# Kernel optimization log

Hardware: AMD Instinct MI355X
Metric: run time of the kernel (lower is better)

The kernel has to match this reference:

```python
import jax, jax.numpy as jnp
import numpy as np

NEG_SLOPE = 0.01  # nn.LeakyReLU default
NUM_GRAPHS = 64


def leaky_relu(x):
    return jnp.where(x >= 0, x, NEG_SLOPE * x)


def gcn_conv(x, edge_index, W, b):
    """PyG GCNConv: add self-loops, symmetric norm, aggregate, + bias."""
    n = x.shape[0]
    h = x @ W  # [N, F]
    loop = jnp.arange(n, dtype=edge_index.dtype)
    src = jnp.concatenate([edge_index[0], loop])
    dst = jnp.concatenate([edge_index[1], loop])
    deg = jax.ops.segment_sum(jnp.ones_like(dst, dtype=h.dtype), dst, num_segments=n)
    dinv = jnp.where(deg > 0, deg ** -0.5, 0.0)
    norm = dinv[src] * dinv[dst]  # [E+N]
    msg = h[src] * norm[:, None]  # [E+N, F] dominant intermediate
    out = jax.ops.segment_sum(msg, dst, num_segments=n)
    return out + b


def gep(x, batch, num_graphs):
    """global mean pool over batch segment ids."""
    s = jax.ops.segment_sum(x, batch, num_segments=num_graphs)
    cnt = jax.ops.segment_sum(jnp.ones(x.shape[0], dtype=x.dtype), batch, num_segments=num_graphs)
    return s / jnp.maximum(cnt, 1.0)[:, None]


def setup_inputs() -> dict:
    key = jax.random.key(0)
    ks = jax.random.split(key, 16)
    N, E, F, D, B = 10000, 80000, 1024, 128, NUM_GRAPHS
    sc = 1.0 / np.sqrt(F)
    inp = {
        "pro1_x": jax.random.normal(ks[0], (N, F), jnp.float32),
        "pro1_edge_index": jax.random.randint(ks[1], (2, E), 0, N, jnp.int64),
        "pro1_batch": jnp.sort(jax.random.randint(ks[2], (N,), 0, B, jnp.int64)),
        "pro2_x": jax.random.normal(ks[3], (N, F), jnp.float32),
        "pro2_edge_index": jax.random.randint(ks[4], (2, E), 0, N, jnp.int64),
        "pro2_batch": jnp.sort(jax.random.randint(ks[5], (N,), 0, B, jnp.int64)),
        "mas1_straight": 0, "mas1_flipped": 0, "mas2_straight": 0, "mas2_flipped": 0,
        "conv1_W": jax.random.normal(ks[6], (F, F), jnp.float32) * sc,
        "conv1_b": jnp.zeros((F,), jnp.float32),
        "fc1_W": jax.random.normal(ks[7], (F, D), jnp.float32) * sc,
        "fc1_b": jnp.zeros((D,), jnp.float32),
        "conv2_W": jax.random.normal(ks[8], (F, F), jnp.float32) * sc,
        "conv2_b": jnp.zeros((F,), jnp.float32),
        "fc2_W": jax.random.normal(ks[9], (F, D), jnp.float32) * sc,
        "fc2_b": jnp.zeros((D,), jnp.float32),
        "final_W": jax.random.normal(ks[10], (2 * D, 1), jnp.float32) * (1.0 / np.sqrt(2 * D)),
        "final_b": jnp.zeros((1,), jnp.float32),
    }
    return inp


def reference(pro1_x, pro1_edge_index, pro1_batch, pro2_x, pro2_edge_index, pro2_batch,
              mas1_straight, mas1_flipped, mas2_straight, mas2_flipped,
              conv1_W, conv1_b, fc1_W, fc1_b, conv2_W, conv2_b, fc2_W, fc2_b,
              final_W, final_b):
    # branch 1 (dropout = identity at inference)
    x = leaky_relu(gcn_conv(pro1_x, pro1_edge_index, conv1_W, conv1_b))
    x = gep(x, pro1_batch, NUM_GRAPHS)
    x = leaky_relu(x @ fc1_W + fc1_b)
    # branch 2
    xt = leaky_relu(gcn_conv(pro2_x, pro2_edge_index, conv2_W, conv2_b))
    xt = gep(xt, pro2_batch, NUM_GRAPHS)
    xt = leaky_relu(xt @ fc2_W + fc2_b)
    combined = jnp.concatenate([x, xt], axis=1)  # [B, 256]
    return combined @ final_W + final_b  # [B, 1]
```

## Files before the change

kernel.cpp:

```cpp
#include <hip/hip_runtime.h>
#include <cstdint>
#include <cstddef>

#define FDIM 1024
#define DDIM 128
#define NGRAPH 64
#define FCH 8
#define QN 4
#define FILLB 320

#define AS1 __attribute__((address_space(1)))
#define AS3 __attribute__((address_space(3)))

typedef float f32x4 __attribute__((ext_vector_type(4)));
typedef short s16x8 __attribute__((ext_vector_type(8)));

__device__ __forceinline__ unsigned short f2bf(float f) {
  unsigned int x = __float_as_uint(f);
  unsigned int r = (x + 0x7fffu + ((x >> 16) & 1u)) >> 16;
  return (unsigned short)r;
}
__device__ __forceinline__ float bflo(unsigned int v) {
  return __uint_as_float(v << 16);
}
__device__ __forceinline__ float bfhi(unsigned int v) {
  return __uint_as_float(v & 0xffff0000u);
}

__device__ __forceinline__ int lower_bound(const int* a, int n, int v) {
  int lo = 0, hi = n;
  while (lo < hi) {
    int mid = (lo + hi) >> 1;
    if (a[mid] < v) lo = mid + 1; else hi = mid;
  }
  return lo;
}
__global__ __launch_bounds__(256) void k_init(int* deg1, int* deg2,
                                              const int* __restrict__ batch1,
                                              const int* __restrict__ batch2,
                                              int* cnt1, int* gstart1,
                                              int* cnt2, int* gstart2, int N) {
  int bid = blockIdx.x, t = threadIdx.x;
  if (bid < 40) {
    int i = bid * 256 + t;
    if (i < N) deg1[i] = 1;
  } else if (bid < 80) {
    int i = (bid - 40) * 256 + t;
    if (i < N) deg2[i] = 1;
  } else {
    if (t < 128) {
      const int* batch = (t < NGRAPH) ? batch1 : batch2;
      int* cnt = (t < NGRAPH) ? cnt1 : cnt2;
      int* gstart = (t < NGRAPH) ? gstart1 : gstart2;
      int g = t & (NGRAPH - 1);
      int lo = lower_bound(batch, N, g);
      int hi = lower_bound(batch, N, g + 1);
      gstart[g] = lo;
      cnt[g] = hi - lo;
    }
  }
}

__global__ __launch_bounds__(256) void k_prep_cast(const int* __restrict__ ei1,
                                                   const int* __restrict__ ei2,
                                                   int* deg1, int* deg2,
                                                   const float4* __restrict__ x1,
                                                   const float4* __restrict__ x2,
                                                   const float* __restrict__ W1,
                                                   const float* __restrict__ W2,
                                                   ushort4* xb1, ushort4* xb2,
                                                   unsigned short* Wt1, unsigned short* Wt2,
                                                   int E, int n4, int gE, int nxb) {
  __shared__ unsigned short tile[64][65];
  int br = blockIdx.y;
  int x = blockIdx.x, t = threadIdx.x;
  if (x < gE) {
    const int* ei = br ? ei2 : ei1;
    int* deg = br ? deg2 : deg1;
    int i = x * 256 + t;
    if (i < E) atomicAdd(&deg[ei[E + i]], 1);
  } else if (x < gE + nxb) {
    const float4* xx = br ? x2 : x1;
    ushort4* xb = br ? xb2 : xb1;
    int i = (x - gE) * 256 + t;
    if (i < n4) {
      float4 v = xx[i];
      ushort4 o;
      o.x = f2bf(v.x); o.y = f2bf(v.y); o.z = f2bf(v.z); o.w = f2bf(v.w);
      xb[i] = o;
    }
  } else {
    const float* W = br ? W2 : W1;
    unsigned short* Wt = br ? Wt2 : Wt1;
    int tid16 = x - gE - nxb;
    int kb = tid16 >> 4, nb = tid16 & 15;
    int tn = t & 63, tg = t >> 6;
    #pragma unroll
    for (int r = 0; r < 16; ++r) {
      int kk = tg * 16 + r;
      tile[kk][tn] = f2bf(W[(size_t)(kb * 64 + kk) * FDIM + nb * 64 + tn]);
    }
    __syncthreads();
    #pragma unroll
    for (int r = 0; r < 16; ++r) {
      int nn = tg * 16 + r;
      Wt[(size_t)(nb * 64 + nn) * FDIM + kb * 64 + tn] = tile[tn][nn];
    }
  }
}

#define SCAN_T 1024
#define SCAN_PER 16
__global__ __launch_bounds__(SCAN_T) void k_scan(const int* __restrict__ deg1,
                                                 const int* __restrict__ deg2,
                                                 int* off1, int* off2,
                                                 int* cur1, int* cur2,
                                                 float* dinv1, float* dinv2, int n) {
  const int* deg = blockIdx.x ? deg2 : deg1;
  int* off = blockIdx.x ? off2 : off1;
  int* cur = blockIdx.x ? cur2 : cur1;
  float* dinv = blockIdx.x ? dinv2 : dinv1;
  __shared__ int sums[SCAN_T];
  int t = threadIdx.x;
  int base = t * SCAN_PER;
  int local[SCAN_PER];
  int s = 0;
  #pragma unroll
  for (int i = 0; i < SCAN_PER; ++i) {
    int idx = base + i;
    int d = (idx < n) ? deg[idx] : 0;
    local[i] = s;
    s += d;
    if (idx < n) dinv[idx] = rsqrtf((float)d);
  }
  sums[t] = s;
  __syncthreads();
  for (int o = 1; o < SCAN_T; o <<= 1) {
    int v = (t >= o) ? sums[t - o] : 0;
    __syncthreads();
    sums[t] += v;
    __syncthreads();
  }
  int basesum = (t > 0) ? sums[t - 1] : 0;
  #pragma unroll
  for (int i = 0; i < SCAN_PER; ++i) {
    int idx = base + i;
    if (idx < n) { int o = basesum + local[i]; off[idx] = o; cur[idx] = o; }
  }
  if (t == SCAN_T - 1) off[n] = sums[SCAN_T - 1];
}

__global__ __launch_bounds__(256) void k_fill_gemm(const int* __restrict__ ei1,
                                                   const int* __restrict__ ei2,
                                                   int* cur1, int* cur2,
                                                   const float* __restrict__ dinv1,
                                                   const float* __restrict__ dinv2,
                                                   int* adjsrc1, int* adjsrc2,
                                                   float* adjw1, float* adjw2,
                                                   const unsigned short* __restrict__ A1,
                                                   const unsigned short* __restrict__ A2,
                                                   const unsigned short* __restrict__ B1,
                                                   const unsigned short* __restrict__ B2,
                                                   unsigned short* __restrict__ C1,
                                                   unsigned short* __restrict__ C2,
                                                   int E, int N, int M) {
  __shared__ unsigned short sm[8192];
  int br = blockIdx.y;
  if (blockIdx.x < FILLB) {
    const int* ei = br ? ei2 : ei1;
    int* cur = br ? cur2 : cur1;
    const float* dinv = br ? dinv2 : dinv1;
    int* adjsrc = br ? adjsrc2 : adjsrc1;
    float* adjw = br ? adjw2 : adjw1;
    int i = blockIdx.x * 256 + threadIdx.x;
    if (i < E) {
      int s = ei[i];
      int d = ei[E + i];
      int p = atomicAdd(&cur[d], 1);
      adjsrc[p] = s;
      adjw[p] = dinv[s] * dinv[d];
    }
    if (i < N) {
      int p = atomicAdd(&cur[i], 1);
      adjsrc[p] = i;
      adjw[p] = dinv[i] * dinv[i];
    }
    return;
  }
  const unsigned short* A = br ? A2 : A1;
  const unsigned short* Bt = br ? B2 : B1;
  unsigned short* C = br ? C2 : C1;
  const int K = FDIM;
  int tid = threadIdx.x;
  int w = tid >> 6, lane = tid & 63;
  int wm = w >> 1, wn = w & 1;

  int bx = blockIdx.x - FILLB;
  int per_xcd = (gridDim.x - FILLB) >> 3;
  int l = (bx & 7) * per_xcd + (bx >> 3);
  int m0 = (l >> 3) * 128;
  int n0 = (l & 7) * 128;

  int sub = lane >> 2;
  int kq = lane & 3;

  f32x4 acc[4][4];
  #pragma unroll
  for (int i = 0; i < 4; ++i)
    #pragma unroll
    for (int j = 0; j < 4; ++j)
      acc[i][j] = (f32x4){0.f, 0.f, 0.f, 0.f};

  for (int k0 = 0; k0 < K; k0 += 32) {
    #pragma unroll
    for (int j = 0; j < 2; ++j) {
      int chunk = w * 2 + j;
      int ra = m0 + chunk * 16 + sub;
      if (ra > M - 1) ra = M - 1;
      const unsigned short* ga = A + (size_t)ra * K + k0 + kq * 8;
      __builtin_amdgcn_global_load_lds((const AS1 unsigned int*)ga,
                                       (AS3 unsigned int*)&sm[chunk * 512], 16, 0, 0);
      int rb = n0 + chunk * 16 + sub;
      const unsigned short* gb = Bt + (size_t)rb * K + k0 + kq * 8;
      __builtin_amdgcn_global_load_lds((const AS1 unsigned int*)gb,
                                       (AS3 unsigned int*)&sm[4096 + chunk * 512], 16, 0, 0);
    }
    __syncthreads();
    s16x8 af[4], bfr[4];
    #pragma unroll
    for (int i = 0; i < 4; ++i) {
      int rowa = wm * 64 + i * 16 + (lane & 15);
      af[i] = *(const s16x8*)&sm[rowa * 32 + (lane >> 4) * 8];
      int rowb = wn * 64 + i * 16 + (lane & 15);
      bfr[i] = *(const s16x8*)&sm[4096 + rowb * 32 + (lane >> 4) * 8];
    }
    #pragma unroll
    for (int i = 0; i < 4; ++i)
      #pragma unroll
      for (int j = 0; j < 4; ++j)
        acc[i][j] = __builtin_amdgcn_mfma_f32_16x16x32_bf16(af[i], bfr[j], acc[i][j], 0, 0, 0);
    __syncthreads();
  }

  #pragma unroll
  for (int i = 0; i < 4; ++i) {
    int row_base = m0 + wm * 64 + i * 16 + (lane >> 4) * 4;
    #pragma unroll
    for (int j = 0; j < 4; ++j) {
      int col = n0 + wn * 64 + j * 16 + (lane & 15);
      #pragma unroll
      for (int r = 0; r < 4; ++r) {
        int row = row_base + r;
        if (row < M) C[(size_t)row * FDIM + col] = f2bf(acc[i][j][r]);
      }
    }
  }
}

__global__ __launch_bounds__(256) void k_aggpool(const unsigned short* __restrict__ h1,
                                                 const unsigned short* __restrict__ h2,
                                                 const int* __restrict__ off1,
                                                 const int* __restrict__ off2,
                                                 const int* __restrict__ adjsrc1,
                                                 const int* __restrict__ adjsrc2,
                                                 const float* __restrict__ adjw1,
                                                 const float* __restrict__ adjw2,
                                                 const float* __restrict__ bias1,
                                                 const float* __restrict__ bias2,
                                                 const int* __restrict__ cnt1,
                                                 const int* __restrict__ cnt2,
                                                 const int* __restrict__ gstart1,
                                                 const int* __restrict__ gstart2,
                                                 float* pool4_1, float* pool4_2) {
  int br = blockIdx.y;
  const unsigned short* h = br ? h2 : h1;
  const int* off = br ? off2 : off1;
  const int* adjsrc = br ? adjsrc2 : adjsrc1;
  const float* adjw = br ? adjw2 : adjw1;
  const float* bias = br ? bias2 : bias1;
  const int* cnt = br ? cnt2 : cnt1;
  const int* gstart = br ? gstart2 : gstart1;
  float* pool4 = br ? pool4_2 : pool4_1;

  int x = blockIdx.x;
  int chunk = x & (FCH - 1);
  int r = x >> 3;
  int g = r & (NGRAPH - 1);
  int q = r >> 6;

  int t = threadIdx.x;
  int grp = t >> 6, lane = t & 63;

  int n = cnt[g];
  int start = gstart[g];
  int per = (n + QN - 1) / QN;
  int v0 = start + q * per;
  int v1 = min(start + n, v0 + per);

  int colbase = chunk * 128 + lane * 2;
  const unsigned short* hc = h + colbase;
  float2 b2 = *(const float2*)(bias + colbase);
  float s0 = 0.f, s1 = 0.f;

  for (int v = v0 + grp; v < v1; v += 4) {
    int pb = off[v], pe = off[v + 1];
    float a0 = 0.f, a1 = 0.f;
    for (int pbb = pb; pbb < pe; pbb += 64) {
      int m = min(64, pe - pbb);
      int lp = pbb + ((lane < m) ? lane : (m - 1));
      int vs = adjsrc[lp];
      float vw = adjw[lp];
      int j = 0;
      for (; j + 4 <= m; j += 4) {
        int i0 = __shfl(vs, j),     i1 = __shfl(vs, j + 1);
        int i2 = __shfl(vs, j + 2), i3 = __shfl(vs, j + 3);
        float w0 = __shfl(vw, j),     w1 = __shfl(vw, j + 1);
        float w2 = __shfl(vw, j + 2), w3 = __shfl(vw, j + 3);
        unsigned int h0 = *(const unsigned int*)(hc + ((size_t)i0 << 10));
        unsigned int hv1 = *(const unsigned int*)(hc + ((size_t)i1 << 10));
        unsigned int hv2 = *(const unsigned int*)(hc + ((size_t)i2 << 10));
        unsigned int hv3 = *(const unsigned int*)(hc + ((size_t)i3 << 10));
        a0 += w0 * bflo(h0);  a1 += w0 * bfhi(h0);
        a0 += w1 * bflo(hv1); a1 += w1 * bfhi(hv1);
        a0 += w2 * bflo(hv2); a1 += w2 * bfhi(hv2);
        a0 += w3 * bflo(hv3); a1 += w3 * bfhi(hv3);
      }
      for (; j < m; ++j) {
        int i0 = __shfl(vs, j);
        float w0 = __shfl(vw, j);
        unsigned int h0 = *(const unsigned int*)(hc + ((size_t)i0 << 10));
        a0 += w0 * bflo(h0);
        a1 += w0 * bfhi(h0);
      }
    }
    a0 += b2.x; a1 += b2.y;
    s0 += (a0 >= 0.f) ? a0 : 0.01f * a0;
    s1 += (a1 >= 0.f) ? a1 : 0.01f * a1;
  }

  __shared__ float sm[4][128];
  sm[grp][lane * 2] = s0;
  sm[grp][lane * 2 + 1] = s1;
  __syncthreads();
  if (t < 128) {
    float sum = sm[0][t] + sm[1][t] + sm[2][t] + sm[3][t];
    float ic = 1.0f / fmaxf((float)n, 1.0f);
    pool4[((size_t)(q * NGRAPH + g)) * FDIM + chunk * 128 + t] = sum * ic;
  }
}

__global__ __launch_bounds__(DDIM) void k_fc(const float* __restrict__ pool4_1,
                                             const float* __restrict__ pool4_2,
                                             const float* __restrict__ W1,
                                             const float* __restrict__ W2,
                                             const float* __restrict__ b1,
                                             const float* __restrict__ b2,
                                             float* out1, float* out2) {
  const float* pool4 = blockIdx.y ? pool4_2 : pool4_1;
  const float* W = blockIdx.y ? W2 : W1;
  const float* b = blockIdx.y ? b2 : b1;
  float* out = blockIdx.y ? out2 : out1;
  int g = blockIdx.x;
  int j = threadIdx.x;
  __shared__ float xs[FDIM];
  for (int k = j; k < FDIM; k += DDIM) {
    float v = 0.f;
    #pragma unroll
    for (int q = 0; q < QN; ++q)
      v += pool4[((size_t)(q * NGRAPH + g)) * FDIM + k];
    xs[k] = v;
  }
  __syncthreads();
  float acc = b[j];
  for (int k = 0; k < FDIM; ++k) acc += xs[k] * W[(size_t)k * DDIM + j];
  out[g * DDIM + j] = (acc >= 0.f) ? acc : 0.01f * acc;
}

__global__ __launch_bounds__(DDIM) void k_final(const float* __restrict__ o1,
                                                const float* __restrict__ o2,
                                                const float* __restrict__ W,
                                                const float* __restrict__ b,
                                                float* __restrict__ out) {
  int g = blockIdx.x;
  int t = threadIdx.x;
  float acc = o1[g * DDIM + t] * W[t] + o2[g * DDIM + t] * W[DDIM + t];
  #pragma unroll
  for (int o = 32; o > 0; o >>= 1) acc += __shfl_down(acc, o);
  __shared__ float ws2[2];
  if ((t & 63) == 0) ws2[t >> 6] = acc;
  __syncthreads();
  if (t == 0) out[g] = ws2[0] + ws2[1] + b[0];
}

extern "C" void kernel_launch(void* const* d_in, const int* in_sizes, int n_in,
                              void* d_out, int out_size, void* d_ws, size_t ws_size,
                              hipStream_t stream) {
  const float* x1 = (const float*)d_in[0];
  const int* ei1 = (const int*)d_in[1];
  const int* batch1 = (const int*)d_in[2];
  const float* x2 = (const float*)d_in[3];
  const int* ei2 = (const int*)d_in[4];
  const int* batch2 = (const int*)d_in[5];
  const float* conv1_W = (const float*)d_in[10];
  const float* conv1_b = (const float*)d_in[11];
  const float* fc1_W = (const float*)d_in[12];
  const float* fc1_b = (const float*)d_in[13];
  const float* conv2_W = (const float*)d_in[14];
  const float* conv2_b = (const float*)d_in[15];
  const float* fc2_W = (const float*)d_in[16];
  const float* fc2_b = (const float*)d_in[17];
  const float* final_W = (const float*)d_in[18];
  const float* final_b = (const float*)d_in[19];
  float* out = (float*)d_out;

  const int N = in_sizes[2];
  const int E = in_sizes[1] / 2;
  const int A = E + N;

  size_t off_b = 0;
  auto alloc = [&](size_t bytes) -> void* {
    void* p = (char*)d_ws + off_b;
    off_b += (bytes + 255) & ~(size_t)255;
    return p;
  };
  unsigned short* xbf1 = (unsigned short*)alloc((size_t)N * FDIM * 2);
  unsigned short* xbf2 = (unsigned short*)alloc((size_t)N * FDIM * 2);
  unsigned short* hbf1 = (unsigned short*)alloc((size_t)N * FDIM * 2);
  unsigned short* hbf2 = (unsigned short*)alloc((size_t)N * FDIM * 2);
  unsigned short* Wt1 = (unsigned short*)alloc((size_t)FDIM * FDIM * 2);
  unsigned short* Wt2 = (unsigned short*)alloc((size_t)FDIM * FDIM * 2);
  int* deg1 = (int*)alloc(N * 4);
  int* deg2 = (int*)alloc(N * 4);
  int* cnt1 = (int*)alloc(NGRAPH * 4);
  int* cnt2 = (int*)alloc(NGRAPH * 4);
  int* gstart1 = (int*)alloc(NGRAPH * 4);
  int* gstart2 = (int*)alloc(NGRAPH * 4);
  int* off1 = (int*)alloc((N + 1) * 4);
  int* off2 = (int*)alloc((N + 1) * 4);
  int* cur1 = (int*)alloc(N * 4);
  int* cur2 = (int*)alloc(N * 4);
  float* dinv1 = (float*)alloc(N * 4);
  float* dinv2 = (float*)alloc(N * 4);
  int* adjsrc1 = (int*)alloc((size_t)A * 4);
  int* adjsrc2 = (int*)alloc((size_t)A * 4);
  float* adjw1 = (float*)alloc((size_t)A * 4);
  float* adjw2 = (float*)alloc((size_t)A * 4);
  float* pool4_1 = (float*)alloc((size_t)QN * NGRAPH * FDIM * 4);
  float* pool4_2 = (float*)alloc((size_t)QN * NGRAPH * FDIM * 4);
  float* fco1 = (float*)alloc(NGRAPH * DDIM * 4);
  float* fco2 = (float*)alloc(NGRAPH * DDIM * 4);

  const int T = 256;
  int gE = (E + T - 1) / T;
  int n4 = N * FDIM / 4;
  int nxb = (n4 + T - 1) / T;
  int mt = (N + 127) / 128;
  dim3 gPrepCast(gE + nxb + 256, 2);
  dim3 gFillGemm(FILLB + mt * 8, 2);
  dim3 gAgg(FCH * NGRAPH * QN, 2);
  dim3 gFc(NGRAPH, 2);

  k_init<<<81, T, 0, stream>>>(deg1, deg2, batch1, batch2,
                               cnt1, gstart1, cnt2, gstart2, N);
  k_prep_cast<<<gPrepCast, T, 0, stream>>>(ei1, ei2, deg1, deg2,
                                           (const float4*)x1, (const float4*)x2,
                                           conv1_W, conv2_W,
                                           (ushort4*)xbf1, (ushort4*)xbf2, Wt1, Wt2,
                                           E, n4, gE, nxb);
  k_scan<<<2, SCAN_T, 0, stream>>>(deg1, deg2, off1, off2, cur1, cur2, dinv1, dinv2, N);
  k_fill_gemm<<<gFillGemm, T, 0, stream>>>(ei1, ei2, cur1, cur2, dinv1, dinv2,
                                           adjsrc1, adjsrc2, adjw1, adjw2,
                                           xbf1, xbf2, Wt1, Wt2, hbf1, hbf2,
                                           E, N, N);
  k_aggpool<<<gAgg, T, 0, stream>>>(hbf1, hbf2, off1, off2, adjsrc1, adjsrc2,
                                    adjw1, adjw2, conv1_b, conv2_b,
                                    cnt1, cnt2, gstart1, gstart2, pool4_1, pool4_2);
  k_fc<<<gFc, DDIM, 0, stream>>>(pool4_1, pool4_2, fc1_W, fc2_W, fc1_b, fc2_b, fco1, fco2);
  k_final<<<NGRAPH, DDIM, 0, stream>>>(fco1, fco2, final_W, final_b, out);
}
```

Baseline: 334.4 us.

## Enlarge GEMM tiles, fuse fc+final, fold init into scan, widen cast

The bf16 MFMA GEMM moves from 128x128x32 tiles to 256x128x64 tiles with 8x4 accumulators per wave and a larger LDS buffer, raising data reuse per global load. The k_init kernel is replaced by memsets plus a third scan block that computes graph boundaries, with the self-loop degree added inside the scan. The fc and final kernels are fused into one launch, and the x cast now writes 8 bf16 values per thread. This cuts launches and intermediate buffers, at the cost of higher register and LDS pressure in the GEMM that may reduce occupancy.

New measurement: 341.3 us. +2.1%, slower.

```diff
diff --git a/kernel.cpp b/kernel.cpp
--- a/kernel.cpp
+++ b/kernel.cpp
@@ -9,11 +9,16 @@
 #define QN 4
 #define FILLB 320
 
+#define BM 256
+#define BN 128
+#define BK 64
+
 #define AS1 __attribute__((address_space(1)))
 #define AS3 __attribute__((address_space(3)))
 
 typedef float f32x4 __attribute__((ext_vector_type(4)));
 typedef short s16x8 __attribute__((ext_vector_type(8)));
+typedef unsigned short u16x8 __attribute__((ext_vector_type(8)));
 
 __device__ __forceinline__ unsigned short f2bf(float f) {
   unsigned int x = __float_as_uint(f);
@@ -34,31 +39,6 @@
     if (a[mid] < v) lo = mid + 1; else hi = mid;
   }
   return lo;
-}
-__global__ __launch_bounds__(256) void k_init(int* deg1, int* deg2,
-                                              const int* __restrict__ batch1,
-                                              const int* __restrict__ batch2,
-                                              int* cnt1, int* gstart1,
-                                              int* cnt2, int* gstart2, int N) {
-  int bid = blockIdx.x, t = threadIdx.x;
-  if (bid < 40) {
-    int i = bid * 256 + t;
-    if (i < N) deg1[i] = 1;
-  } else if (bid < 80) {
-    int i = (bid - 40) * 256 + t;
-    if (i < N) deg2[i] = 1;
-  } else {
-    if (t < 128) {
-      const int* batch = (t < NGRAPH) ? batch1 : batch2;
-      int* cnt = (t < NGRAPH) ? cnt1 : cnt2;
-      int* gstart = (t < NGRAPH) ? gstart1 : gstart2;
-      int g = t & (NGRAPH - 1);
-      int lo = lower_bound(batch, N, g);
-      int hi = lower_bound(batch, N, g + 1);
-      gstart[g] = lo;
-      cnt[g] = hi - lo;
-    }
-  }
 }
 
 __global__ __launch_bounds__(256) void k_prep_cast(const int* __restrict__ ei1,
@@ -68,9 +48,9 @@
                                                    const float4* __restrict__ x2,
                                                    const float* __restrict__ W1,
                                                    const float* __restrict__ W2,
-                                                   ushort4* xb1, ushort4* xb2,
+                                                   u16x8* xb1, u16x8* xb2,
                                                    unsigned short* Wt1, unsigned short* Wt2,
-                                                   int E, int n4, int gE, int nxb) {
+                                                   int E, int n8, int gE, int nxb) {
   __shared__ unsigned short tile[64][65];
   int br = blockIdx.y;
   int x = blockIdx.x, t = threadIdx.x;
@@ -81,12 +61,14 @@
     if (i < E) atomicAdd(&deg[ei[E + i]], 1);
   } else if (x < gE + nxb) {
     const float4* xx = br ? x2 : x1;
-    ushort4* xb = br ? xb2 : xb1;
+    u16x8* xb = br ? xb2 : xb1;
     int i = (x - gE) * 256 + t;
-    if (i < n4) {
-      float4 v = xx[i];
-      ushort4 o;
-      o.x = f2bf(v.x); o.y = f2bf(v.y); o.z = f2bf(v.z); o.w = f2bf(v.w);
+    if (i < n8) {
+      float4 v0 = xx[2 * i];
+      float4 v1 = xx[2 * i + 1];
+      u16x8 o;
+      o[0] = f2bf(v0.x); o[1] = f2bf(v0.y); o[2] = f2bf(v0.z); o[3] = f2bf(v0.w);
+      o[4] = f2bf(v1.x); o[5] = f2bf(v1.y); o[6] = f2bf(v1.z); o[7] = f2bf(v1.w);
       xb[i] = o;
     }
   } else {
@@ -115,7 +97,25 @@
                                                  const int* __restrict__ deg2,
                                                  int* off1, int* off2,
                                                  int* cur1, int* cur2,
-                                                 float* dinv1, float* dinv2, int n) {
+                                                 float* dinv1, float* dinv2,
+                                                 const int* __restrict__ batch1,
+                                                 const int* __restrict__ batch2,
+                                                 int* cnt1, int* gstart1,
+                                                 int* cnt2, int* gstart2, int n) {
+  if (blockIdx.x == 2) {
+    int t = threadIdx.x;
+    if (t < 128) {
+      const int* batch = (t < NGRAPH) ? batch1 : batch2;
+      int* cnt = (t < NGRAPH) ? cnt1 : cnt2;
+      int* gstart = (t < NGRAPH) ? gstart1 : gstart2;
+      int g = t & (NGRAPH - 1);
+      int lo = lower_bound(batch, n, g);
+      int hi = lower_bound(batch, n, g + 1);
+      gstart[g] = lo;
+      cnt[g] = hi - lo;
+    }
+    return;
+  }
   const int* deg = blockIdx.x ? deg2 : deg1;
   int* off = blockIdx.x ? off2 : off1;
   int* cur = blockIdx.x ? cur2 : cur1;
@@ -128,7 +128,7 @@
   #pragma unroll
   for (int i = 0; i < SCAN_PER; ++i) {
     int idx = base + i;
-    int d = (idx < n) ? deg[idx] : 0;
+    int d = (idx < n) ? (deg[idx] + 1) : 0;
     local[i] = s;
     s += d;
     if (idx < n) dinv[idx] = rsqrtf((float)d);
@@ -150,21 +150,21 @@
   if (t == SCAN_T - 1) off[n] = sums[SCAN_T - 1];
 }
 
-__global__ __launch_bounds__(256) void k_fill_gemm(const int* __restrict__ ei1,
-                                                   const int* __restrict__ ei2,
-                                                   int* cur1, int* cur2,
-                                                   const float* __restrict__ dinv1,
-                                                   const float* __restrict__ dinv2,
-                                                   int* adjsrc1, int* adjsrc2,
-                                                   float* adjw1, float* adjw2,
-                                                   const unsigned short* __restrict__ A1,
-                                                   const unsigned short* __restrict__ A2,
-                                                   const unsigned short* __restrict__ B1,
-                                                   const unsigned short* __restrict__ B2,
-                                                   unsigned short* __restrict__ C1,
-                                                   unsigned short* __restrict__ C2,
-                                                   int E, int N, int M) {
-  __shared__ unsigned short sm[8192];
+__global__ __launch_bounds__(256, 2) void k_fill_gemm(const int* __restrict__ ei1,
+                                                      const int* __restrict__ ei2,
+                                                      int* cur1, int* cur2,
+                                                      const float* __restrict__ dinv1,
+                                                      const float* __restrict__ dinv2,
+                                                      int* adjsrc1, int* adjsrc2,
+                                                      float* adjw1, float* adjw2,
+                                                      const unsigned short* __restrict__ A1,
+                                                      const unsigned short* __restrict__ A2,
+                                                      const unsigned short* __restrict__ B1,
+                                                      const unsigned short* __restrict__ B2,
+                                                      unsigned short* __restrict__ C1,
+                                                      unsigned short* __restrict__ C2,
+                                                      int E, int N, int M) {
+  __shared__ unsigned short sm[24576];
   int br = blockIdx.y;
   if (blockIdx.x < FILLB) {
     const int* ei = br ? ei2 : ei1;
@@ -198,53 +198,61 @@
   int bx = blockIdx.x - FILLB;
   int per_xcd = (gridDim.x - FILLB) >> 3;
   int l = (bx & 7) * per_xcd + (bx >> 3);
-  int m0 = (l >> 3) * 128;
-  int n0 = (l & 7) * 128;
-
-  int sub = lane >> 2;
-  int kq = lane & 3;
-
-  f32x4 acc[4][4];
+  int m0 = (l >> 3) * BM;
+  int n0 = (l & 7) * BN;
+
+  int seg_r = lane >> 3;
+  int seg_c = lane & 7;
+
+  f32x4 acc[8][4];
   #pragma unroll
-  for (int i = 0; i < 4; ++i)
+  for (int i = 0; i < 8; ++i)
     #pragma unroll
     for (int j = 0; j < 4; ++j)
       acc[i][j] = (f32x4){0.f, 0.f, 0.f, 0.f};
 
-  for (int k0 = 0; k0 < K; k0 += 32) {
-    #pragma unroll
-    for (int j = 0; j < 2; ++j) {
-      int chunk = w * 2 + j;
-      int ra = m0 + chunk * 16 + sub;
+  for (int k0 = 0; k0 < K; k0 += BK) {
+    #pragma unroll
+    for (int c = 0; c < 8; ++c) {
+      int ra = m0 + c * 32 + w * 8 + seg_r;
       if (ra > M - 1) ra = M - 1;
-      const unsigned short* ga = A + (size_t)ra * K + k0 + kq * 8;
+      const unsigned short* ga = A + (size_t)ra * K + k0 + seg_c * 8;
       __builtin_amdgcn_global_load_lds((const AS1 unsigned int*)ga,
-                                       (AS3 unsigned int*)&sm[chunk * 512], 16, 0, 0);
-      int rb = n0 + chunk * 16 + sub;
-      const unsigned short* gb = Bt + (size_t)rb * K + k0 + kq * 8;
+                                       (AS3 unsigned int*)&sm[c * 2048 + w * 512], 16, 0, 0);
+    }
+    #pragma unroll
+    for (int c = 0; c < 4; ++c) {
+      int rb = n0 + c * 32 + w * 8 + seg_r;
+      const unsigned short* gb = Bt + (size_t)rb * K + k0 + seg_c * 8;
       __builtin_amdgcn_global_load_lds((const AS1 unsigned int*)gb,
-                                       (AS3 unsigned int*)&sm[4096 + chunk * 512], 16, 0, 0);
+                                       (AS3 unsigned int*)&sm[16384 + c * 2048 + w * 512], 16, 0, 0);
     }
     __syncthreads();
-    s16x8 af[4], bfr[4];
-    #pragma unroll
-    for (int i = 0; i < 4; ++i) {
-      int rowa = wm * 64 + i * 16 + (lane & 15);
-      af[i] = *(const s16x8*)&sm[rowa * 32 + (lane >> 4) * 8];
-      int rowb = wn * 64 + i * 16 + (lane & 15);
-      bfr[i] = *(const s16x8*)&sm[4096 + rowb * 32 + (lane >> 4) * 8];
-    }
-    #pragma unroll
-    for (int i = 0; i < 4; ++i)
+    #pragma unroll
+    for (int kk = 0; kk < 2; ++kk) {
+      s16x8 af[8], bfr[4];
       #pragma unroll
-      for (int j = 0; j < 4; ++j)
-        acc[i][j] = __builtin_amdgcn_mfma_f32_16x16x32_bf16(af[i], bfr[j], acc[i][j], 0, 0, 0);
+      for (int i = 0; i < 8; ++i) {
+        int rowa = wm * 128 + i * 16 + (lane & 15);
+        af[i] = *(const s16x8*)&sm[rowa * 64 + kk * 32 + (lane >> 4) * 8];
+      }
+      #pragma unroll
+      for (int j = 0; j < 4; ++j) {
+        int rowb = wn * 64 + j * 16 + (lane & 15);
+        bfr[j] = *(const s16x8*)&sm[16384 + rowb * 64 + kk * 32 + (lane >> 4) * 8];
+      }
+      #pragma unroll
+      for (int i = 0; i < 8; ++i)
+        #pragma unroll
+        for (int j = 0; j < 4; ++j)
+          acc[i][j] = __builtin_amdgcn_mfma_f32_16x16x32_bf16(af[i], bfr[j], acc[i][j], 0, 0, 0);
+    }
     __syncthreads();
   }
 
   #pragma unroll
-  for (int i = 0; i < 4; ++i) {
-    int row_base = m0 + wm * 64 + i * 16 + (lane >> 4) * 4;
+  for (int i = 0; i < 8; ++i) {
+    int row_base = m0 + wm * 128 + i * 16 + (lane >> 4) * 4;
     #pragma unroll
     for (int j = 0; j < 4; ++j) {
       int col = n0 + wn * 64 + j * 16 + (lane & 15);
@@ -349,47 +357,41 @@
   }
 }
 
-__global__ __launch_bounds__(DDIM) void k_fc(const float* __restrict__ pool4_1,
-                                             const float* __restrict__ pool4_2,
-                                             const float* __restrict__ W1,
-                                             const float* __restrict__ W2,
-                                             const float* __restrict__ b1,
-                                             const float* __restrict__ b2,
-                                             float* out1, float* out2) {
-  const float* pool4 = blockIdx.y ? pool4_2 : pool4_1;
-  const float* W = blockIdx.y ? W2 : W1;
-  const float* b = blockIdx.y ? b2 : b1;
-  float* out = blockIdx.y ? out2 : out1;
+__global__ __launch_bounds__(256) void k_fc_final(const float* __restrict__ pool4_1,
+                                                  const float* __restrict__ pool4_2,
+                                                  const float* __restrict__ W1,
+                                                  const float* __restrict__ W2,
+                                                  const float* __restrict__ b1,
+                                                  const float* __restrict__ b2,
+                                                  const float* __restrict__ fW,
+                                                  const float* __restrict__ fb,
+                                                  float* __restrict__ out) {
   int g = blockIdx.x;
-  int j = threadIdx.x;
-  __shared__ float xs[FDIM];
+  int t = threadIdx.x;
+  int half = t >> 7;
+  int j = t & 127;
+  const float* pool4 = half ? pool4_2 : pool4_1;
+  const float* W = half ? W2 : W1;
+  const float* b = half ? b2 : b1;
+  __shared__ float xs[2][FDIM];
   for (int k = j; k < FDIM; k += DDIM) {
     float v = 0.f;
     #pragma unroll
     for (int q = 0; q < QN; ++q)
       v += pool4[((size_t)(q * NGRAPH + g)) * FDIM + k];
-    xs[k] = v;
+    xs[half][k] = v;
   }
   __syncthreads();
   float acc = b[j];
-  for (int k = 0; k < FDIM; ++k) acc += xs[k] * W[(size_t)k * DDIM + j];
-  out[g * DDIM + j] = (acc >= 0.f) ? acc : 0.01f * acc;
-}
-
-__global__ __launch_bounds__(DDIM) void k_final(const float* __restrict__ o1,
-                                                const float* __restrict__ o2,
-                                                const float* __restrict__ W,
-                                                const float* __restrict__ b,
-                                                float* __restrict__ out) {
-  int g = blockIdx.x;
-  int t = threadIdx.x;
-  float acc = o1[g * DDIM + t] * W[t] + o2[g * DDIM + t] * W[DDIM + t];
+  for (int k = 0; k < FDIM; ++k) acc += xs[half][k] * W[(size_t)k * DDIM + j];
+  acc = (acc >= 0.f) ? acc : 0.01f * acc;
+  float c = acc * fW[half * DDIM + j];
   #pragma unroll
-  for (int o = 32; o > 0; o >>= 1) acc += __shfl_down(acc, o);
-  __shared__ float ws2[2];
-  if ((t & 63) == 0) ws2[t >> 6] = acc;
+  for (int o = 32; o > 0; o >>= 1) c += __shfl_down(c, o);
+  __shared__ float ws[4];
+  if ((t & 63) == 0) ws[t >> 6] = c;
   __syncthreads();
-  if (t == 0) out[g] = ws2[0] + ws2[1] + b[0];
+  if (t == 0) out[g] = ws[0] + ws[1] + ws[2] + ws[3] + fb[0];
 }
 
 extern "C" void kernel_launch(void* const* d_in, const int* in_sizes, int n_in,
@@ -447,27 +449,25 @@
   float* adjw2 = (float*)alloc((size_t)A * 4);
   float* pool4_1 = (float*)alloc((size_t)QN * NGRAPH * FDIM * 4);
   float* pool4_2 = (float*)alloc((size_t)QN * NGRAPH * FDIM * 4);
-  float* fco1 = (float*)alloc(NGRAPH * DDIM * 4);
-  float* fco2 = (float*)alloc(NGRAPH * DDIM * 4);
 
   const int T = 256;
   int gE = (E + T - 1) / T;
-  int n4 = N * FDIM / 4;
-  int nxb = (n4 + T - 1) / T;
-  int mt = (N + 127) / 128;
+  int n8 = N * FDIM / 8;
+  int nxb = (n8 + T - 1) / T;
+  int mt = (N + BM - 1) / BM;
   dim3 gPrepCast(gE + nxb + 256, 2);
   dim3 gFillGemm(FILLB + mt * 8, 2);
   dim3 gAgg(FCH * NGRAPH * QN, 2);
-  dim3 gFc(NGRAPH, 2);
-
-  k_init<<<81, T, 0, stream>>>(deg1, deg2, batch1, batch2,
-                               cnt1, gstart1, cnt2, gstart2, N);
+
+  hipMemsetAsync(deg1, 0, (size_t)N * 4, stream);
+  hipMemsetAsync(deg2, 0, (size_t)N * 4, stream);
   k_prep_cast<<<gPrepCast, T, 0, stream>>>(ei1, ei2, deg1, deg2,
                                            (const float4*)x1, (const float4*)x2,
                                            conv1_W, conv2_W,
-                                           (ushort4*)xbf1, (ushort4*)xbf2, Wt1, Wt2,
-                                           E, n4, gE, nxb);
-  k_scan<<<2, SCAN_T, 0, stream>>>(deg1, deg2, off1, off2, cur1, cur2, dinv1, dinv2, N);
+                                           (u16x8*)xbf1, (u16x8*)xbf2, Wt1, Wt2,
+                                           E, n8, gE, nxb);
+  k_scan<<<3, SCAN_T, 0, stream>>>(deg1, deg2, off1, off2, cur1, cur2, dinv1, dinv2,
+                                   batch1, batch2, cnt1, gstart1, cnt2, gstart2, N);
   k_fill_gemm<<<gFillGemm, T, 0, stream>>>(ei1, ei2, cur1, cur2, dinv1, dinv2,
                                            adjsrc1, adjsrc2, adjw1, adjw2,
                                            xbf1, xbf2, Wt1, Wt2, hbf1, hbf2,
@@ -475,6 +475,6 @@
   k_aggpool<<<gAgg, T, 0, stream>>>(hbf1, hbf2, off1, off2, adjsrc1, adjsrc2,
                                     adjw1, adjw2, conv1_b, conv2_b,
                                     cnt1, cnt2, gstart1, gstart2, pool4_1, pool4_2);
-  k_fc<<<gFc, DDIM, 0, stream>>>(pool4_1, pool4_2, fc1_W, fc2_W, fc1_b, fc2_b, fco1, fco2);
-  k_final<<<NGRAPH, DDIM, 0, stream>>>(fco1, fco2, final_W, final_b, out);
-}
+  k_fc_final<<<NGRAPH, T, 0, stream>>>(pool4_1, pool4_2, fc1_W, fc2_W, fc1_b, fc2_b,
+                                       final_W, final_b, out);
+}
```
